# Performance work log

Measured on AMD Instinct MI355X. Metric: run time of the kernel, lower is better.

Reference implementation:

```python
import jax, jax.numpy as jnp
import numpy as np

N_NODES = 50000
N_EDGES = 800000
D_MODEL = 128
N_HEADS = 8
D_HEAD = D_MODEL // N_HEADS


def _layernorm(x, g, b, eps=1e-5):
    mu = jnp.mean(x, axis=-1, keepdims=True)
    var = jnp.mean(jnp.square(x - mu), axis=-1, keepdims=True)
    return (x - mu) * jax.lax.rsqrt(var + eps) * g + b


def setup_inputs() -> dict:
    key = jax.random.key(0)
    ks = jax.random.split(key, 8)
    x = jax.random.normal(ks[0], (N_NODES, D_MODEL), dtype=jnp.float32)
    edge_attr = jax.random.normal(ks[1], (N_EDGES, N_HEADS, D_HEAD), dtype=jnp.float32)
    s = 1.0 / np.sqrt(D_MODEL)
    qkv_w = jax.random.normal(ks[2], (D_MODEL, 3 * D_MODEL), dtype=jnp.float32) * s
    qkv_b = jax.random.normal(ks[3], (3 * D_MODEL,), dtype=jnp.float32) * 0.01
    out_w = jax.random.normal(ks[4], (D_MODEL, D_MODEL), dtype=jnp.float32) * s
    out_b = jax.random.normal(ks[5], (D_MODEL,), dtype=jnp.float32) * 0.01
    ln_g = jnp.ones((D_MODEL,), dtype=jnp.float32)
    ln_b = jnp.zeros((D_MODEL,), dtype=jnp.float32)
    edge_index = jax.random.randint(ks[6], (2, N_EDGES), 0, N_NODES, dtype=jnp.int64)
    return {"x": x, "edge_attr": edge_attr, "qkv_w": qkv_w, "qkv_b": qkv_b,
            "out_w": out_w, "out_b": out_b, "ln_g": ln_g, "ln_b": ln_b,
            "edge_index": edge_index}


def reference(x, edge_attr, qkv_w, qkv_b, out_w, out_b, ln_g, ln_b, edge_index):
    N, C = x.shape
    h = _layernorm(x, ln_g, ln_b)  # pre-norm
    qkv = (h @ qkv_w + qkv_b).reshape(N, 3, N_HEADS, D_HEAD)
    q, k, v = qkv[:, 0], qkv[:, 1], qkv[:, 2]  # each [N, H, D]
    src, dst = edge_index[0], edge_index[1]    # PyG: j = source, i = target
    # edge-wise attention logits [E, H]
    scores = jnp.sum(q[dst] * (k[src] + edge_attr), axis=-1) * (D_HEAD ** -0.5)
    # segment softmax over target index
    m = jax.ops.segment_max(scores, dst, num_segments=N)          # [N, H]
    m = jnp.where(jnp.isfinite(m), m, 0.0)
    e = jnp.exp(scores - m[dst])                                   # [E, H]
    s = jax.ops.segment_sum(e, dst, num_segments=N)                # [N, H]
    attn = e / jnp.maximum(s[dst], 1e-16)                          # [E, H]
    msg = v[src] * attn[:, :, None]                                # [E, H, D]
    agg = jax.ops.segment_sum(msg, dst, num_segments=N)            # [N, H, D]
    out = agg.reshape(N, C) @ out_w + out_b
    return x + out
```

## Files before the change

kernel.cpp:

```cpp
#include <hip/hip_runtime.h>

#define NN 50000
#define NE 800000

__global__ __launch_bounds__(256) void ln_qkv(
    const float* __restrict__ x, const float* __restrict__ g,
    const float* __restrict__ b, const float* __restrict__ W,
    const float* __restrict__ bias, float* __restrict__ Out, int M) {
  const int Nw = 384;
  int row  = blockIdx.x * 256 + threadIdx.x;
  int n0   = blockIdx.y * 64;
  bool live = row < M;
  const float* xr = x + (size_t)(live ? row : 0) * 128;

  float sum = 0.f, sq = 0.f;
  for (int k = 0; k < 128; k += 4) {
    float4 a = *(const float4*)(xr + k);
    sum += a.x + a.y + a.z + a.w;
    sq  += a.x * a.x + a.y * a.y + a.z * a.z + a.w * a.w;
  }
  float mu  = sum * (1.f / 128.f);
  float var = sq * (1.f / 128.f) - mu * mu;
  float inv = rsqrtf(var + 1e-5f);

  float acc[64];
#pragma unroll
  for (int j = 0; j < 64; ++j) acc[j] = 0.f;

  for (int k = 0; k < 128; k += 4) {
    float4 a  = *(const float4*)(xr + k);
    float4 gg = *(const float4*)(g + k);
    float4 bb = *(const float4*)(b + k);
    float an[4];
    an[0] = (a.x - mu) * inv * gg.x + bb.x;
    an[1] = (a.y - mu) * inv * gg.y + bb.y;
    an[2] = (a.z - mu) * inv * gg.z + bb.z;
    an[3] = (a.w - mu) * inv * gg.w + bb.w;
#pragma unroll
    for (int t = 0; t < 4; ++t) {
      float ak = an[t];
      const float* wr = W + (size_t)(k + t) * Nw + n0;
#pragma unroll
      for (int j = 0; j < 16; ++j) {
        float4 w = *(const float4*)(wr + 4 * j);
        acc[4 * j + 0] += ak * w.x;
        acc[4 * j + 1] += ak * w.y;
        acc[4 * j + 2] += ak * w.z;
        acc[4 * j + 3] += ak * w.w;
      }
    }
  }

  if (!live) return;
  float* o = Out + (size_t)row * Nw + n0;
#pragma unroll
  for (int j = 0; j < 16; ++j) {
    float4 bb = *(const float4*)(bias + n0 + 4 * j);
    float4 ov;
    ov.x = acc[4 * j + 0] + bb.x;
    ov.y = acc[4 * j + 1] + bb.y;
    ov.z = acc[4 * j + 2] + bb.z;
    ov.w = acc[4 * j + 3] + bb.w;
    *(float4*)(o + 4 * j) = ov;
  }
}

__global__ __launch_bounds__(256) void gemm_rw(
    const float* __restrict__ A, const float* __restrict__ W,
    const float* __restrict__ bias, const float* __restrict__ resid,
    float* __restrict__ Out, int M, int Nw) {
  int row  = blockIdx.x * 256 + threadIdx.x;
  int n0   = blockIdx.y * 64;
  bool live = row < M;
  const float* Ar = A + (size_t)(live ? row : 0) * 128;

  float acc[64];
#pragma unroll
  for (int j = 0; j < 64; ++j) acc[j] = 0.f;

  for (int k = 0; k < 128; k += 4) {
    float4 a4 = *(const float4*)(Ar + k);
#pragma unroll
    for (int t = 0; t < 4; ++t) {
      float ak = (t == 0) ? a4.x : (t == 1) ? a4.y : (t == 2) ? a4.z : a4.w;
      const float* wr = W + (size_t)(k + t) * Nw + n0;
#pragma unroll
      for (int j = 0; j < 16; ++j) {
        float4 w = *(const float4*)(wr + 4 * j);
        acc[4 * j + 0] += ak * w.x;
        acc[4 * j + 1] += ak * w.y;
        acc[4 * j + 2] += ak * w.z;
        acc[4 * j + 3] += ak * w.w;
      }
    }
  }

  if (!live) return;
  float* o = Out + (size_t)row * Nw + n0;
  const float* r = resid + (size_t)row * Nw + n0;
#pragma unroll
  for (int j = 0; j < 16; ++j) {
    float4 bb = *(const float4*)(bias + n0 + 4 * j);
    float4 rv = *(const float4*)(r + 4 * j);
    float4 ov;
    ov.x = acc[4 * j + 0] + bb.x + rv.x;
    ov.y = acc[4 * j + 1] + bb.y + rv.y;
    ov.z = acc[4 * j + 2] + bb.z + rv.z;
    ov.w = acc[4 * j + 3] + bb.w + rv.w;
    *(float4*)(o + 4 * j) = ov;
  }
}

__global__ __launch_bounds__(256) void count_kernel(
    const int* __restrict__ ei, int* __restrict__ cnt, int E) {
  int e = blockIdx.x * blockDim.x + threadIdx.x;
  if (e >= E) return;
  atomicAdd(&cnt[ei[E + e]], 1);
}

__global__ __launch_bounds__(256) void block_sums(
    const int* __restrict__ cnt, int* __restrict__ bsum, int n) {
  int i = blockIdx.x * 256 + threadIdx.x;
  int v = (i < n) ? cnt[i] : 0;
#pragma unroll
  for (int o = 32; o > 0; o >>= 1) v += __shfl_down(v, o);
  __shared__ int ws[4];
  if ((threadIdx.x & 63) == 0) ws[threadIdx.x >> 6] = v;
  __syncthreads();
  if (threadIdx.x == 0) bsum[blockIdx.x] = ws[0] + ws[1] + ws[2] + ws[3];
}

__global__ __launch_bounds__(256) void scan_write(
    const int* __restrict__ cnt, const int* __restrict__ bsum,
    int* __restrict__ row_start, int* __restrict__ cursor, int n, int total) {
  __shared__ int wred[4];
  __shared__ int wsum[4];
  __shared__ int off_s;
  int b = blockIdx.x, tid = threadIdx.x;

  int v = (tid < b) ? bsum[tid] : 0;
#pragma unroll
  for (int o = 32; o > 0; o >>= 1) v += __shfl_down(v, o);
  if ((tid & 63) == 0) wred[tid >> 6] = v;
  __syncthreads();
  if (tid == 0) off_s = wred[0] + wred[1] + wred[2] + wred[3];

  int i = b * 256 + tid;
  int c = (i < n) ? cnt[i] : 0;
  int xv = c;
#pragma unroll
  for (int o = 1; o < 64; o <<= 1) {
    int t = __shfl_up(xv, o);
    if ((tid & 63) >= o) xv += t;
  }
  if ((tid & 63) == 63) wsum[tid >> 6] = xv;
  __syncthreads();

  int w = tid >> 6;
  int woff = off_s;
  if (w > 0) woff += wsum[0];
  if (w > 1) woff += wsum[1];
  if (w > 2) woff += wsum[2];
  int excl = woff + xv - c;
  if (i < n) {
    row_start[i] = excl;
    cursor[i]    = excl;
  }
  if (i == 0) row_start[n] = total;
}

__global__ __launch_bounds__(256) void scatter_kernel(
    const int* __restrict__ ei, int* __restrict__ cursor,
    int* __restrict__ perm, int E) {
  int e = blockIdx.x * blockDim.x + threadIdx.x;
  if (e >= E) return;
  int pos = atomicAdd(&cursor[ei[E + e]], 1);
  perm[pos] = e;
}

__global__ __launch_bounds__(256) void fused_attn(
    const float* __restrict__ qkv, const float* __restrict__ edge_attr,
    const int* __restrict__ ei, const int* __restrict__ row_start,
    const int* __restrict__ perm, float* __restrict__ agg, int N, int E) {
  int node = (blockIdx.x * blockDim.x + threadIdx.x) >> 6;
  if (node >= N) return;
  int lane = threadIdx.x & 63;
  int ch   = lane * 2;

  float2 q2 = *(const float2*)(qkv + (size_t)node * 384 + ch);

  float m = -INFINITY, l = 0.f;
  float2 acc = make_float2(0.f, 0.f);

  int beg  = row_start[node];
  int stop = row_start[node + 1];

  for (int c0 = beg; c0 < stop; c0 += 64) {
    int nc = min(64, stop - c0);
    int el = 0, sl = 0;
    if (c0 + lane < stop) {
      el = perm[c0 + lane];
      sl = ei[el];
    }
    int j = 0;
    for (; j + 4 <= nc; j += 4) {
      int e0 = __shfl(el, j),     e1 = __shfl(el, j + 1);
      int e2 = __shfl(el, j + 2), e3 = __shfl(el, j + 3);
      int s0 = __shfl(sl, j),     s1 = __shfl(sl, j + 1);
      int s2 = __shfl(sl, j + 2), s3 = __shfl(sl, j + 3);
      float2 k0 = *(const float2*)(qkv + (size_t)s0 * 384 + 128 + ch);
      float2 k1 = *(const float2*)(qkv + (size_t)s1 * 384 + 128 + ch);
      float2 k2 = *(const float2*)(qkv + (size_t)s2 * 384 + 128 + ch);
      float2 k3 = *(const float2*)(qkv + (size_t)s3 * 384 + 128 + ch);
      float2 a0 = *(const float2*)(edge_attr + (size_t)e0 * 128 + ch);
      float2 a1 = *(const float2*)(edge_attr + (size_t)e1 * 128 + ch);
      float2 a2 = *(const float2*)(edge_attr + (size_t)e2 * 128 + ch);
      float2 a3 = *(const float2*)(edge_attr + (size_t)e3 * 128 + ch);
      float2 v0 = *(const float2*)(qkv + (size_t)s0 * 384 + 256 + ch);
      float2 v1 = *(const float2*)(qkv + (size_t)s1 * 384 + 256 + ch);
      float2 v2 = *(const float2*)(qkv + (size_t)s2 * 384 + 256 + ch);
      float2 v3 = *(const float2*)(qkv + (size_t)s3 * 384 + 256 + ch);
      float p0 = q2.x * (k0.x + a0.x) + q2.y * (k0.y + a0.y);
      float p1 = q2.x * (k1.x + a1.x) + q2.y * (k1.y + a1.y);
      float p2 = q2.x * (k2.x + a2.x) + q2.y * (k2.y + a2.y);
      float p3 = q2.x * (k3.x + a3.x) + q2.y * (k3.y + a3.y);
      p0 += __shfl_xor(p0, 1); p1 += __shfl_xor(p1, 1);
      p2 += __shfl_xor(p2, 1); p3 += __shfl_xor(p3, 1);
      p0 += __shfl_xor(p0, 2); p1 += __shfl_xor(p1, 2);
      p2 += __shfl_xor(p2, 2); p3 += __shfl_xor(p3, 2);
      p0 += __shfl_xor(p0, 4); p1 += __shfl_xor(p1, 4);
      p2 += __shfl_xor(p2, 4); p3 += __shfl_xor(p3, 4);
      float sc0 = p0 * 0.25f, sc1 = p1 * 0.25f;
      float sc2 = p2 * 0.25f, sc3 = p3 * 0.25f;
      float mn = fmaxf(fmaxf(fmaxf(m, sc0), fmaxf(sc1, sc2)), sc3);
      float scale = __expf(m - mn);
      float pe0 = __expf(sc0 - mn), pe1 = __expf(sc1 - mn);
      float pe2 = __expf(sc2 - mn), pe3 = __expf(sc3 - mn);
      l = l * scale + pe0 + pe1 + pe2 + pe3;
      acc.x = acc.x * scale + pe0 * v0.x + pe1 * v1.x + pe2 * v2.x + pe3 * v3.x;
      acc.y = acc.y * scale + pe0 * v0.y + pe1 * v1.y + pe2 * v2.y + pe3 * v3.y;
      m = mn;
    }
    for (; j < nc; ++j) {
      int e0 = __shfl(el, j);
      int s0 = __shfl(sl, j);
      float2 kv = *(const float2*)(qkv + (size_t)s0 * 384 + 128 + ch);
      float2 ea = *(const float2*)(edge_attr + (size_t)e0 * 128 + ch);
      float2 vv = *(const float2*)(qkv + (size_t)s0 * 384 + 256 + ch);
      float p = q2.x * (kv.x + ea.x) + q2.y * (kv.y + ea.y);
      p += __shfl_xor(p, 1);
      p += __shfl_xor(p, 2);
      p += __shfl_xor(p, 4);
      float s  = p * 0.25f;
      float mn = fmaxf(m, s);
      float scale = __expf(m - mn);
      float pe    = __expf(s - mn);
      l = l * scale + pe;
      acc.x = acc.x * scale + pe * vv.x;
      acc.y = acc.y * scale + pe * vv.y;
      m = mn;
    }
  }
  float inv = 1.f / fmaxf(l, 1e-16f);
  float2 o = make_float2(acc.x * inv, acc.y * inv);
  *(float2*)(agg + (size_t)node * 128 + ch) = o;
}

extern "C" void kernel_launch(void* const* d_in, const int* in_sizes, int n_in,
                              void* d_out, int out_size, void* d_ws,
                              size_t ws_size, hipStream_t stream) {
  const float* x         = (const float*)d_in[0];
  const float* edge_attr = (const float*)d_in[1];
  const float* qkv_w     = (const float*)d_in[2];
  const float* qkv_b     = (const float*)d_in[3];
  const float* out_w     = (const float*)d_in[4];
  const float* out_b     = (const float*)d_in[5];
  const float* ln_g      = (const float*)d_in[6];
  const float* ln_b      = (const float*)d_in[7];
  const int*   ei        = (const int*)d_in[8];
  float* out = (float*)d_out;

  const int N = NN, E = NE;
  const int NB = (N + 255) / 256;
  float* qkv       = (float*)d_ws;
  float* agg       = qkv + (size_t)N * 384;
  int*   cnt       = (int*)(agg + (size_t)N * 128);
  int*   bsum      = cnt + N;
  int*   row_start = bsum + 256;
  int*   cursor    = row_start + N + 1;
  int*   perm      = cursor + N;

  hipMemsetAsync(cnt, 0, (size_t)N * 4, stream);
  count_kernel<<<(E + 255) / 256, 256, 0, stream>>>(ei, cnt, E);
  block_sums<<<NB, 256, 0, stream>>>(cnt, bsum, N);
  scan_write<<<NB, 256, 0, stream>>>(cnt, bsum, row_start, cursor, N, E);
  scatter_kernel<<<(E + 255) / 256, 256, 0, stream>>>(ei, cursor, perm, E);

  dim3 g1(NB, 384 / 64);
  ln_qkv<<<g1, 256, 0, stream>>>(x, ln_g, ln_b, qkv_w, qkv_b, qkv, N);

  fused_attn<<<(N * 64 + 255) / 256, 256, 0, stream>>>(
      qkv, edge_attr, ei, row_start, perm, agg, N, E);

  dim3 g2(NB, 128 / 64);
  gemm_rw<<<g2, 256, 0, stream>>>(agg, out_w, out_b, x, out, N, 128);
}
```

Baseline: 908.2 us.

## Restructure edge attention: per-lane edge scoring, packed CSR adjacency, lazy max rescale

The scatter kernel now writes packed (src, edge) pairs, so the attention kernel no longer does a dependent ei[perm] lookup. In the attention kernel each 8-lane head group scores 8 different edges at once. Each lane computes a full 16-wide dot product with float4 loads, which removes the per-edge shuffle reductions for the dot product. The running max is only rescaled when some score exceeds it by more than 8, which skips most exp rescales. V accumulation still broadcasts each edge's source and weight and loads float2 per lane, and the memory access pattern for K and edge_attr changes to 64-byte contiguous reads per lane.

```diff
diff --git a/kernel.cpp b/kernel.cpp
--- a/kernel.cpp
+++ b/kernel.cpp
@@ -171,23 +171,28 @@
 
 __global__ __launch_bounds__(256) void scatter_kernel(
     const int* __restrict__ ei, int* __restrict__ cursor,
-    int* __restrict__ perm, int E) {
+    int2* __restrict__ adj, int E) {
   int e = blockIdx.x * blockDim.x + threadIdx.x;
   if (e >= E) return;
   int pos = atomicAdd(&cursor[ei[E + e]], 1);
-  perm[pos] = e;
+  adj[pos] = make_int2(ei[e], e);
 }
 
 __global__ __launch_bounds__(256) void fused_attn(
     const float* __restrict__ qkv, const float* __restrict__ edge_attr,
-    const int* __restrict__ ei, const int* __restrict__ row_start,
-    const int* __restrict__ perm, float* __restrict__ agg, int N, int E) {
+    const int2* __restrict__ adj, const int* __restrict__ row_start,
+    float* __restrict__ agg, int N) {
   int node = (blockIdx.x * blockDim.x + threadIdx.x) >> 6;
   if (node >= N) return;
   int lane = threadIdx.x & 63;
-  int ch   = lane * 2;
-
-  float2 q2 = *(const float2*)(qkv + (size_t)node * 384 + ch);
+  int h = lane >> 3, t = lane & 7;
+  int ch = lane * 2;
+
+  const float* qb = qkv + (size_t)node * 384 + h * 16;
+  float4 q0 = *(const float4*)(qb + 0);
+  float4 q1 = *(const float4*)(qb + 4);
+  float4 q2 = *(const float4*)(qb + 8);
+  float4 q3 = *(const float4*)(qb + 12);
 
   float m = -INFINITY, l = 0.f;
   float2 acc = make_float2(0.f, 0.f);
@@ -197,68 +202,67 @@
 
   for (int c0 = beg; c0 < stop; c0 += 64) {
     int nc = min(64, stop - c0);
-    int el = 0, sl = 0;
-    if (c0 + lane < stop) {
-      el = perm[c0 + lane];
-      sl = ei[el];
+    int sl = 0, el = 0;
+    if (lane < nc) {
+      int2 ae = adj[c0 + lane];
+      sl = ae.x;
+      el = ae.y;
     }
-    int j = 0;
-    for (; j + 4 <= nc; j += 4) {
-      int e0 = __shfl(el, j),     e1 = __shfl(el, j + 1);
-      int e2 = __shfl(el, j + 2), e3 = __shfl(el, j + 3);
-      int s0 = __shfl(sl, j),     s1 = __shfl(sl, j + 1);
-      int s2 = __shfl(sl, j + 2), s3 = __shfl(sl, j + 3);
-      float2 k0 = *(const float2*)(qkv + (size_t)s0 * 384 + 128 + ch);
-      float2 k1 = *(const float2*)(qkv + (size_t)s1 * 384 + 128 + ch);
-      float2 k2 = *(const float2*)(qkv + (size_t)s2 * 384 + 128 + ch);
-      float2 k3 = *(const float2*)(qkv + (size_t)s3 * 384 + 128 + ch);
-      float2 a0 = *(const float2*)(edge_attr + (size_t)e0 * 128 + ch);
-      float2 a1 = *(const float2*)(edge_attr + (size_t)e1 * 128 + ch);
-      float2 a2 = *(const float2*)(edge_attr + (size_t)e2 * 128 + ch);
-      float2 a3 = *(const float2*)(edge_attr + (size_t)e3 * 128 + ch);
-      float2 v0 = *(const float2*)(qkv + (size_t)s0 * 384 + 256 + ch);
-      float2 v1 = *(const float2*)(qkv + (size_t)s1 * 384 + 256 + ch);
-      float2 v2 = *(const float2*)(qkv + (size_t)s2 * 384 + 256 + ch);
-      float2 v3 = *(const float2*)(qkv + (size_t)s3 * 384 + 256 + ch);
-      float p0 = q2.x * (k0.x + a0.x) + q2.y * (k0.y + a0.y);
-      float p1 = q2.x * (k1.x + a1.x) + q2.y * (k1.y + a1.y);
-      float p2 = q2.x * (k2.x + a2.x) + q2.y * (k2.y + a2.y);
-      float p3 = q2.x * (k3.x + a3.x) + q2.y * (k3.y + a3.y);
-      p0 += __shfl_xor(p0, 1); p1 += __shfl_xor(p1, 1);
-      p2 += __shfl_xor(p2, 1); p3 += __shfl_xor(p3, 1);
-      p0 += __shfl_xor(p0, 2); p1 += __shfl_xor(p1, 2);
-      p2 += __shfl_xor(p2, 2); p3 += __shfl_xor(p3, 2);
-      p0 += __shfl_xor(p0, 4); p1 += __shfl_xor(p1, 4);
-      p2 += __shfl_xor(p2, 4); p3 += __shfl_xor(p3, 4);
-      float sc0 = p0 * 0.25f, sc1 = p1 * 0.25f;
-      float sc2 = p2 * 0.25f, sc3 = p3 * 0.25f;
-      float mn = fmaxf(fmaxf(fmaxf(m, sc0), fmaxf(sc1, sc2)), sc3);
-      float scale = __expf(m - mn);
-      float pe0 = __expf(sc0 - mn), pe1 = __expf(sc1 - mn);
-      float pe2 = __expf(sc2 - mn), pe3 = __expf(sc3 - mn);
-      l = l * scale + pe0 + pe1 + pe2 + pe3;
-      acc.x = acc.x * scale + pe0 * v0.x + pe1 * v1.x + pe2 * v2.x + pe3 * v3.x;
-      acc.y = acc.y * scale + pe0 * v0.y + pe1 * v1.y + pe2 * v2.y + pe3 * v3.y;
-      m = mn;
-    }
-    for (; j < nc; ++j) {
-      int e0 = __shfl(el, j);
-      int s0 = __shfl(sl, j);
-      float2 kv = *(const float2*)(qkv + (size_t)s0 * 384 + 128 + ch);
-      float2 ea = *(const float2*)(edge_attr + (size_t)e0 * 128 + ch);
-      float2 vv = *(const float2*)(qkv + (size_t)s0 * 384 + 256 + ch);
-      float p = q2.x * (kv.x + ea.x) + q2.y * (kv.y + ea.y);
-      p += __shfl_xor(p, 1);
-      p += __shfl_xor(p, 2);
-      p += __shfl_xor(p, 4);
-      float s  = p * 0.25f;
-      float mn = fmaxf(m, s);
-      float scale = __expf(m - mn);
-      float pe    = __expf(s - mn);
-      l = l * scale + pe;
-      acc.x = acc.x * scale + pe * vv.x;
-      acc.y = acc.y * scale + pe * vv.y;
-      m = mn;
+    for (int j0 = 0; j0 < nc; j0 += 8) {
+      int idx = j0 + t;
+      int sL = __shfl(sl, idx);
+      int eL = __shfl(el, idx);
+      const float* kb = qkv + (size_t)sL * 384 + 128 + h * 16;
+      const float* ab = edge_attr + (size_t)eL * 128 + h * 16;
+      float4 k0 = *(const float4*)(kb + 0);
+      float4 k1 = *(const float4*)(kb + 4);
+      float4 k2 = *(const float4*)(kb + 8);
+      float4 k3 = *(const float4*)(kb + 12);
+      float4 a0 = *(const float4*)(ab + 0);
+      float4 a1 = *(const float4*)(ab + 4);
+      float4 a2 = *(const float4*)(ab + 8);
+      float4 a3 = *(const float4*)(ab + 12);
+      float d;
+      d  = q0.x * (k0.x + a0.x) + q0.y * (k0.y + a0.y) +
+           q0.z * (k0.z + a0.z) + q0.w * (k0.w + a0.w);
+      d += q1.x * (k1.x + a1.x) + q1.y * (k1.y + a1.y) +
+           q1.z * (k1.z + a1.z) + q1.w * (k1.w + a1.w);
+      d += q2.x * (k2.x + a2.x) + q2.y * (k2.y + a2.y) +
+           q2.z * (k2.z + a2.z) + q2.w * (k2.w + a2.w);
+      d += q3.x * (k3.x + a3.x) + q3.y * (k3.y + a3.y) +
+           q3.z * (k3.z + a3.z) + q3.w * (k3.w + a3.w);
+      float s = (idx < nc) ? d * 0.25f : -INFINITY;
+
+      float mx = s;
+      mx = fmaxf(mx, __shfl_xor(mx, 1));
+      mx = fmaxf(mx, __shfl_xor(mx, 2));
+      mx = fmaxf(mx, __shfl_xor(mx, 4));
+
+      if (!__all(mx <= m + 8.f)) {
+        float mn = fmaxf(m, mx);
+        float sc = __expf(m - mn);
+        l *= sc;
+        acc.x *= sc;
+        acc.y *= sc;
+        m = mn;
+      }
+      float pe = __expf(s - m);
+
+      float ls = pe;
+      ls += __shfl_xor(ls, 1);
+      ls += __shfl_xor(ls, 2);
+      ls += __shfl_xor(ls, 4);
+      l += ls;
+
+      int gbase = lane & 56;
+#pragma unroll
+      for (int j = 0; j < 8; ++j) {
+        int sj = __shfl(sL, j);
+        float pj = __shfl(pe, gbase + j);
+        float2 vv = *(const float2*)(qkv + (size_t)sj * 384 + 256 + ch);
+        acc.x += pj * vv.x;
+        acc.y += pj * vv.y;
+      }
     }
   }
   float inv = 1.f / fmaxf(l, 1e-16f);
@@ -288,19 +292,19 @@
   int*   bsum      = cnt + N;
   int*   row_start = bsum + 256;
   int*   cursor    = row_start + N + 1;
-  int*   perm      = cursor + N;
+  int2*  adj       = (int2*)(cursor + N);
 
   hipMemsetAsync(cnt, 0, (size_t)N * 4, stream);
   count_kernel<<<(E + 255) / 256, 256, 0, stream>>>(ei, cnt, E);
   block_sums<<<NB, 256, 0, stream>>>(cnt, bsum, N);
   scan_write<<<NB, 256, 0, stream>>>(cnt, bsum, row_start, cursor, N, E);
-  scatter_kernel<<<(E + 255) / 256, 256, 0, stream>>>(ei, cursor, perm, E);
+  scatter_kernel<<<(E + 255) / 256, 256, 0, stream>>>(ei, cursor, adj, E);
 
   dim3 g1(NB, 384 / 64);
   ln_qkv<<<g1, 256, 0, stream>>>(x, ln_g, ln_b, qkv_w, qkv_b, qkv, N);
 
   fused_attn<<<(N * 64 + 255) / 256, 256, 0, stream>>>(
-      qkv, edge_attr, ei, row_start, perm, agg, N, E);
+      qkv, edge_attr, adj, row_start, agg, N);
 
   dim3 g2(NB, 128 / 64);
   gemm_rw<<<g2, 256, 0, stream>>>(agg, out_w, out_b, x, out, N, 128);
```

After: 988.3 us. +8.8%, slower.
